# Kernel tuning notes

Measured on AMD Instinct MI355X. Metric: run time of the kernel, lower is better.

## Reference

```python
import jax, jax.numpy as jnp
import numpy as np
from math import gamma, comb

D_POLY = 4
OFFSET = 2
EVAL_MAX = 1.4
N_NODES = 50000
N_EDGES = 800000
IN_FEATS = 256
H_FEATS = 64
NEG_SLOPE = 0.01  # F.leaky_relu / nn.LeakyReLU default


def _beta(a, b):
    return gamma(a) * gamma(b) / gamma(a + b)


def _calculate_theta2(d=D_POLY):
    # Closed-form expansion of sympy poly in calculate_theta2:
    # f(x) = (x/e)^i * (1 - x/e)^(d-i+offset) / (e * Beta(i+1, d+1-i+offset))
    # Returns ascending-order coefficient lists (theta[k] = coeff of x^k).
    e = EVAL_MAX
    thetas = []
    for i in range(OFFSET, d + 1 + OFFSET):
        m = d - i + OFFSET
        B = _beta(i + 1, d + 1 - i + OFFSET)
        c = np.zeros(d + 1 + OFFSET, dtype=np.float64)
        for j in range(m + 1):
            c[i + j] = (1.0 / e) ** i * comb(m, j) * (-1.0 / e) ** j / (e * B)
        thetas.append([float(v) for v in c])
    return thetas


THETAS = _calculate_theta2()


def setup_inputs() -> dict:
    key = jax.random.key(0)
    k1, k2, k3, k4, k5 = jax.random.split(key, 5)
    x = jax.random.normal(k1, (N_NODES, IN_FEATS), dtype=jnp.float32)
    W = jax.random.normal(k2, (IN_FEATS, H_FEATS), dtype=jnp.float32) * 0.05
    b = jax.random.normal(k3, (H_FEATS,), dtype=jnp.float32) * 0.05
    src = jax.random.randint(k4, (N_EDGES,), 0, N_NODES, dtype=jnp.int32)
    dst = jax.random.randint(k5, (N_EDGES,), 0, N_NODES, dtype=jnp.int32)
    return {"x": x, "W": W, "b": b, "src": src, "dst": dst}


def reference(x, W, b, src, dst):
    # BWGNN forward: linear + LeakyReLU, then 5 Beta-wavelet PolyConv filters.
    h = jax.nn.leaky_relu(x @ W + b, NEG_SLOPE)  # [N, H]
    # out_degrees, clamped to 1, then D^{-1/2}
    deg = jax.ops.segment_sum(jnp.ones_like(src, dtype=h.dtype), src, num_segments=N_NODES)
    d_inv = jnp.clip(deg, 1.0) ** -0.5
    d_inv = d_inv[:, None]  # [N, 1]
    outs = []
    for theta in THETAS:
        f = h
        acc = theta[0] * h
        for k in range(1, len(theta)):
            # unnLaplacian: f <- f - D^{-1/2} A^T D^{-1/2} f  (copy_u/sum SpMM)
            msg = jax.ops.segment_sum((f * d_inv)[src], dst, num_segments=N_NODES)
            f = f - msg * d_inv
            acc = acc + theta[k] * f
        outs.append(acc)
    return jnp.concatenate(outs, axis=1)  # [N, 5*H]
```

## Files before the change

### kernel.cpp

```cpp
#include <hip/hip_runtime.h>
#include <math.h>

#define NN 50000
#define NN4 12500
#define NE 800000
#define INF 256
#define HF 64
#define OUTF 320
#define NB4 ((NN4 + 255) / 256)
#define G 128
#define SL (NE / G)

typedef _Float16 half8 __attribute__((ext_vector_type(8)));
typedef float floatx4 __attribute__((ext_vector_type(4)));
typedef float f32x2 __attribute__((ext_vector_type(2)));
typedef float f32x4 __attribute__((ext_vector_type(4)));

static __device__ __forceinline__ unsigned short f2h(float x) {
    _Float16 h = (_Float16)x;
    return *(unsigned short*)&h;
}
static __device__ __forceinline__ float h2f(unsigned short u) {
    _Float16 h = *(_Float16*)&u;
    return (float)h;
}

struct ThetaM { float m[5][7]; };

static void compute_theta(ThetaM& tm) {
    const double e = 1.4;
    auto fact = [](int n) { double r = 1.0; for (int i = 2; i <= n; ++i) r *= i; return r; };
    for (int t = 0; t < 5; ++t) {
        int i = t + 2;
        int mm = 6 - i;
        double B = fact(i) * fact(6 - i) / fact(7);
        for (int k = 0; k < 7; ++k) tm.m[t][k] = 0.f;
        for (int j = 0; j <= mm; ++j) {
            double cb = fact(mm) / (fact(j) * fact(mm - j));
            double v = pow(1.0 / e, (double)i) * cb * pow(-1.0 / e, (double)j) / (e * B);
            tm.m[t][i + j] = (float)v;
        }
    }
}

__global__ __launch_bounds__(64) void zero_kernel(unsigned int* __restrict__ gA,
                                                  unsigned int* __restrict__ gB) {
    if (threadIdx.x < 32) {
        gA[NN * 32 + threadIdx.x] = 0u;
        gB[NN * 32 + threadIdx.x] = 0u;
    }
}

__global__ __launch_bounds__(1024) void hist_kernel(const int* __restrict__ src,
                                                    const int* __restrict__ dst,
                                                    unsigned int* __restrict__ hist_dst,
                                                    unsigned int* __restrict__ hist_src) {
    __shared__ unsigned int h[NN4];
    int b = blockIdx.x;
    const int* arr = (b < G) ? dst : src;
    unsigned int* outp = (b < G) ? hist_dst : hist_src;
    int bb = (b < G) ? b : b - G;
    for (int i = threadIdx.x; i < NN4; i += 1024) h[i] = 0u;
    __syncthreads();
    int base = bb * SL;
    for (int i = threadIdx.x; i < SL; i += 1024) {
        int d = arr[base + i];
        atomicAdd(&h[d >> 2], 1u << ((d & 3) * 8));
    }
    __syncthreads();
    unsigned int* out32 = outp + (size_t)bb * NN4;
    for (int i = threadIdx.x; i < NN4; i += 1024) out32[i] = h[i];
}

__global__ __launch_bounds__(256) void merge_kernel(unsigned int* __restrict__ hist_dst,
                                                    const unsigned int* __restrict__ hist_src,
                                                    int* __restrict__ cnt,
                                                    float* __restrict__ dinv,
                                                    int* __restrict__ partial) {
    __shared__ int s[256];
    int tid = threadIdx.x;
    int t = blockIdx.x * 256 + tid;
    int run0 = 0, run1 = 0, run2 = 0, run3 = 0;
    if (t < NN4) {
        for (int b = 0; b < G; ++b) {
            size_t idx = (size_t)b * NN4 + t;
            unsigned int u = hist_dst[idx];
            hist_dst[idx] = (unsigned int)run0 | ((unsigned int)run1 << 8) |
                            ((unsigned int)run2 << 16) | ((unsigned int)run3 << 24);
            run0 += u & 255u; run1 += (u >> 8) & 255u;
            run2 += (u >> 16) & 255u; run3 += u >> 24;
        }
        *(int4*)&cnt[4 * t] = make_int4(run0, run1, run2, run3);
        int d0 = 0, d1 = 0, d2 = 0, d3 = 0;
        for (int b = 0; b < G; ++b) {
            unsigned int u = hist_src[(size_t)b * NN4 + t];
            d0 += u & 255u; d1 += (u >> 8) & 255u;
            d2 += (u >> 16) & 255u; d3 += u >> 24;
        }
        float e0 = (float)(d0 < 1 ? 1 : d0);
        float e1 = (float)(d1 < 1 ? 1 : d1);
        float e2 = (float)(d2 < 1 ? 1 : d2);
        float e3 = (float)(d3 < 1 ? 1 : d3);
        *(float4*)&dinv[4 * t] = make_float4(1.0f / sqrtf(e0), 1.0f / sqrtf(e1),
                                             1.0f / sqrtf(e2), 1.0f / sqrtf(e3));
    }
    int pad = ((run0 + 3) & ~3) + ((run1 + 3) & ~3) + ((run2 + 3) & ~3) + ((run3 + 3) & ~3);
    s[tid] = pad;
    __syncthreads();
    for (int off = 128; off > 0; off >>= 1) {
        if (tid < off) s[tid] += s[tid + off];
        __syncthreads();
    }
    if (tid == 0) partial[blockIdx.x] = s[0];
}

__global__ __launch_bounds__(256) void scan_partials_kernel(const int* __restrict__ partial,
                                                            int* __restrict__ offsets,
                                                            int* __restrict__ row_ptr) {
    __shared__ int s[256];
    int tid = threadIdx.x;
    s[tid] = (tid < NB4) ? partial[tid] : 0;
    __syncthreads();
    for (int off = 1; off < 256; off <<= 1) {
        int t = (tid >= off) ? s[tid - off] : 0;
        __syncthreads();
        s[tid] += t;
        __syncthreads();
    }
    if (tid < NB4) offsets[tid] = (tid == 0) ? 0 : s[tid - 1];
    if (tid == NB4 - 1) row_ptr[NN] = s[tid];
}

__global__ __launch_bounds__(256) void scan_write_kernel(const int* __restrict__ cnt,
                                                         const int* __restrict__ offsets,
                                                         int* __restrict__ row_ptr,
                                                         int* __restrict__ col) {
    __shared__ int s[256];
    int tid = threadIdx.x;
    int t = blockIdx.x * 256 + tid;
    int4 c = make_int4(0, 0, 0, 0);
    if (t < NN4) c = *(const int4*)&cnt[4 * t];
    int p0 = (c.x + 3) & ~3, p1 = (c.y + 3) & ~3, p2 = (c.z + 3) & ~3, p3 = (c.w + 3) & ~3;
    int csum = p0 + p1 + p2 + p3;
    s[tid] = csum;
    __syncthreads();
    for (int off = 1; off < 256; off <<= 1) {
        int v = (tid >= off) ? s[tid - off] : 0;
        __syncthreads();
        s[tid] += v;
        __syncthreads();
    }
    if (t < NN4) {
        int b0 = offsets[blockIdx.x] + s[tid] - csum;
        int b1 = b0 + p0, b2 = b1 + p1, b3 = b2 + p2;
        *(int4*)&row_ptr[4 * t] = make_int4(b0, b1, b2, b3);
        for (int k = c.x; k < p0; ++k) col[b0 + k] = NN;
        for (int k = c.y; k < p1; ++k) col[b1 + k] = NN;
        for (int k = c.z; k < p2; ++k) col[b2 + k] = NN;
        for (int k = c.w; k < p3; ++k) col[b3 + k] = NN;
    }
}

__global__ __launch_bounds__(1024) void fill_kernel(const int* __restrict__ src,
                                                    const int* __restrict__ dst,
                                                    const unsigned char* __restrict__ hist8,
                                                    const int* __restrict__ row_ptr,
                                                    int* __restrict__ col) {
    __shared__ unsigned int cur[NN4];
    int b = blockIdx.x;
    for (int i = threadIdx.x; i < NN4; i += 1024) cur[i] = 0u;
    __syncthreads();
    int base = b * SL;
    const unsigned char* hrow = hist8 + (size_t)b * NN;
    for (int i = threadIdx.x; i < SL; i += 1024) {
        int d = dst[base + i];
        int sh = (d & 3) * 8;
        unsigned int old = atomicAdd(&cur[d >> 2], 1u << sh);
        int rank = (int)((old >> sh) & 255u);
        int pos = row_ptr[d] + (int)hrow[d] + rank;
        col[pos] = src[base + i];
    }
}

__global__ __launch_bounds__(256) void wprep_kernel(const float* __restrict__ W,
                                                    unsigned short* __restrict__ Wt) {
    int id = blockIdx.x * 256 + threadIdx.x;
    if (id >= HF * INF) return;
    int n = id >> 8;
    int k = id & 255;
    Wt[id] = f2h(W[k * HF + n]);
}

__global__ __launch_bounds__(256) void gemm_kernel(const float* __restrict__ x,
                                                   const unsigned short* __restrict__ Wt,
                                                   const float* __restrict__ b,
                                                   const float* __restrict__ dinv,
                                                   float* __restrict__ f,
                                                   unsigned short* __restrict__ g) {
    __shared__ _Float16 wls[64 * 264];
    __shared__ _Float16 xls[64 * 136];
    int tid = threadIdx.x;
    int row0 = blockIdx.x * 64;
    int wave = tid >> 6;
    int lane = tid & 63;
    int q = lane >> 4;
    int ln = lane & 15;

    {
        const uint4* wg = (const uint4*)Wt;
        for (int i = 0; i < 8; ++i) {
            int l = tid + i * 256;
            int r = l >> 5, c = l & 31;
            *(uint4*)&wls[r * 264 + c * 8] = wg[l];
        }
    }

    floatx4 acc[4] = {{0.f,0.f,0.f,0.f},{0.f,0.f,0.f,0.f},{0.f,0.f,0.f,0.f},{0.f,0.f,0.f,0.f}};

    for (int ch = 0; ch < 2; ++ch) {
        __syncthreads();
        for (int i = 0; i < 8; ++i) {
            int l = tid + i * 256;
            int r = l >> 5, c4 = (l & 31) * 4;
            int grow = row0 + r;
            f32x4 v = {0.f, 0.f, 0.f, 0.f};
            if (grow < NN) v = __builtin_nontemporal_load((const f32x4*)&x[(size_t)grow * INF + ch * 128 + c4]);
            ushort4 hv;
            hv.x = f2h(v[0]); hv.y = f2h(v[1]); hv.z = f2h(v[2]); hv.w = f2h(v[3]);
            *(ushort4*)&xls[r * 136 + c4] = hv;
        }
        __syncthreads();
        int m = wave * 16 + ln;
        #pragma unroll
        for (int kb4 = 0; kb4 < 4; ++kb4) {
            int kb = kb4 * 32;
            half8 a = *(const half8*)&xls[m * 136 + kb + q * 8];
            int kg = ch * 128 + kb + q * 8;
            #pragma unroll
            for (int t = 0; t < 4; ++t) {
                half8 bb = *(const half8*)&wls[(t * 16 + ln) * 264 + kg];
                acc[t] = __builtin_amdgcn_mfma_f32_16x16x32_f16(a, bb, acc[t], 0, 0, 0);
            }
        }
    }

    float bias[4];
    #pragma unroll
    for (int t = 0; t < 4; ++t) bias[t] = b[t * 16 + ln];
    #pragma unroll
    for (int r = 0; r < 4; ++r) {
        int grow = row0 + wave * 16 + q * 4 + r;
        if (grow < NN) {
            float dv = dinv[grow];
            #pragma unroll
            for (int t = 0; t < 4; ++t) {
                float h = acc[t][r] + bias[t];
                h = (h > 0.f) ? h : 0.01f * h;
                int cidx = t * 16 + ln;
                f[(size_t)grow * HF + cidx] = h;
                g[(size_t)grow * HF + cidx] = f2h(h * dv);
            }
        }
    }
}

__global__ __launch_bounds__(256) void prop_kernel(const int* __restrict__ row_ptr,
                                                   const int* __restrict__ col,
                                                   const float* __restrict__ dinv,
                                                   const unsigned int* __restrict__ g_in,
                                                   const float* __restrict__ f_in, int fin_stride,
                                                   float* __restrict__ f_out, int fout_stride,
                                                   unsigned int* __restrict__ g_out) {
    int gidx = blockIdx.x * 256 + threadIdx.x;
    int wid = gidx >> 5;
    int c2 = threadIdx.x & 31;
    if (wid >= NN) return;
    int j   = row_ptr[wid];
    int end = row_ptr[wid + 1];
    float s0 = 0.f, s1 = 0.f;
    for (; j + 8 <= end; j += 8) {
        int4 ca = *(const int4*)&col[j];
        int4 cb = *(const int4*)&col[j + 4];
        unsigned int u0 = g_in[ca.x * 32 + c2];
        unsigned int u1 = g_in[ca.y * 32 + c2];
        unsigned int u2 = g_in[ca.z * 32 + c2];
        unsigned int u3 = g_in[ca.w * 32 + c2];
        unsigned int u4 = g_in[cb.x * 32 + c2];
        unsigned int u5 = g_in[cb.y * 32 + c2];
        unsigned int u6 = g_in[cb.z * 32 + c2];
        unsigned int u7 = g_in[cb.w * 32 + c2];
        s0 += ((h2f(u0 & 0xFFFF) + h2f(u1 & 0xFFFF)) + (h2f(u2 & 0xFFFF) + h2f(u3 & 0xFFFF)))
            + ((h2f(u4 & 0xFFFF) + h2f(u5 & 0xFFFF)) + (h2f(u6 & 0xFFFF) + h2f(u7 & 0xFFFF)));
        s1 += ((h2f(u0 >> 16) + h2f(u1 >> 16)) + (h2f(u2 >> 16) + h2f(u3 >> 16)))
            + ((h2f(u4 >> 16) + h2f(u5 >> 16)) + (h2f(u6 >> 16) + h2f(u7 >> 16)));
    }
    if (j < end) {
        int4 ca = *(const int4*)&col[j];
        unsigned int u0 = g_in[ca.x * 32 + c2];
        unsigned int u1 = g_in[ca.y * 32 + c2];
        unsigned int u2 = g_in[ca.z * 32 + c2];
        unsigned int u3 = g_in[ca.w * 32 + c2];
        s0 += (h2f(u0 & 0xFFFF) + h2f(u1 & 0xFFFF)) + (h2f(u2 & 0xFFFF) + h2f(u3 & 0xFFFF));
        s1 += (h2f(u0 >> 16) + h2f(u1 >> 16)) + (h2f(u2 >> 16) + h2f(u3 >> 16));
    }
    float dv = dinv[wid];
    f32x2 fv = __builtin_nontemporal_load((const f32x2*)&f_in[(size_t)wid * fin_stride + 2 * c2]);
    float fx = fv[0] - s0 * dv;
    float fy = fv[1] - s1 * dv;
    f32x2 ov; ov[0] = fx; ov[1] = fy;
    __builtin_nontemporal_store(ov, (f32x2*)&f_out[(size_t)wid * fout_stride + 2 * c2]);
    if (g_out) g_out[wid * 32 + c2] = (unsigned int)f2h(fx * dv) | ((unsigned int)f2h(fy * dv) << 16);
}

__global__ __launch_bounds__(256) void final_kernel(float* __restrict__ out, ThetaM tm) {
    int idx = blockIdx.x * 256 + threadIdx.x;
    if (idx >= NN * 32) return;
    int n = idx >> 5;
    int c = (idx & 31) * 2;
    f32x2 v[5];
    #pragma unroll
    for (int j = 0; j < 5; ++j)
        v[j] = __builtin_nontemporal_load((const f32x2*)&out[(size_t)n * OUTF + j * HF + c]);
    #pragma unroll
    for (int t = 0; t < 5; ++t) {
        f32x2 o = {0.f, 0.f};
        #pragma unroll
        for (int j = 0; j < 5; ++j) {
            if (j >= t) { o[0] += tm.m[t][j + 2] * v[j][0]; o[1] += tm.m[t][j + 2] * v[j][1]; }
        }
        __builtin_nontemporal_store(o, (f32x2*)&out[(size_t)n * OUTF + t * HF + c]);
    }
}

extern "C" void kernel_launch(void* const* d_in, const int* in_sizes, int n_in,
                              void* d_out, int out_size, void* d_ws, size_t ws_size,
                              hipStream_t stream) {
    const float* x  = (const float*)d_in[0];
    const float* W  = (const float*)d_in[1];
    const float* b  = (const float*)d_in[2];
    const int* src  = (const int*)d_in[3];
    const int* dst  = (const int*)d_in[4];
    float* out = (float*)d_out;

    char* ws = (char*)d_ws;
    size_t off = 0;
    auto alloc = [&](size_t bytes) -> void* {
        void* p = ws + off;
        off += (bytes + 255) & ~(size_t)255;
        return p;
    };
    unsigned int* hist_dst = (unsigned int*)alloc((size_t)G * NN4 * 4);
    unsigned int* hist_src = (unsigned int*)alloc((size_t)G * NN4 * 4);
    int*   cnt     = (int*)alloc((size_t)NN * 4);
    int*   row_ptr = (int*)alloc((size_t)(NN + 1) * 4);
    int*   partial = (int*)alloc((size_t)NB4 * 4);
    int*   offsets = (int*)alloc((size_t)NB4 * 4);
    float* dinv    = (float*)alloc((size_t)NN * 4);
    int*   col     = (int*)alloc((size_t)(NE + 4 * NN) * 4);
    unsigned short* wt = (unsigned short*)alloc((size_t)HF * INF * 2);
    float* fbuf    = (float*)alloc((size_t)NN * HF * 4);
    unsigned short* gA = (unsigned short*)alloc((size_t)(NN + 1) * HF * 2);
    unsigned short* gB = (unsigned short*)alloc((size_t)(NN + 1) * HF * 2);

    zero_kernel<<<1, 64, 0, stream>>>((unsigned int*)gA, (unsigned int*)gB);
    hist_kernel<<<2 * G, 1024, 0, stream>>>(src, dst, hist_dst, hist_src);
    merge_kernel<<<NB4, 256, 0, stream>>>(hist_dst, hist_src, cnt, dinv, partial);
    scan_partials_kernel<<<1, 256, 0, stream>>>(partial, offsets, row_ptr);
    scan_write_kernel<<<NB4, 256, 0, stream>>>(cnt, offsets, row_ptr, col);
    fill_kernel<<<G, 1024, 0, stream>>>(src, dst, (const unsigned char*)hist_dst, row_ptr, col);
    wprep_kernel<<<(HF * INF + 255) / 256, 256, 0, stream>>>(W, wt);
    gemm_kernel<<<(NN + 63) / 64, 256, 0, stream>>>(x, wt, b, dinv, fbuf, gA);

    const int PB = (NN * 32 + 255) / 256;
    prop_kernel<<<PB, 256, 0, stream>>>(row_ptr, col, dinv, (unsigned int*)gA, fbuf, HF, fbuf, HF, (unsigned int*)gB);
    prop_kernel<<<PB, 256, 0, stream>>>(row_ptr, col, dinv, (unsigned int*)gB, fbuf, HF, out + 0 * HF, OUTF, (unsigned int*)gA);
    prop_kernel<<<PB, 256, 0, stream>>>(row_ptr, col, dinv, (unsigned int*)gA, out + 0 * HF, OUTF, out + 1 * HF, OUTF, (unsigned int*)gB);
    prop_kernel<<<PB, 256, 0, stream>>>(row_ptr, col, dinv, (unsigned int*)gB, out + 1 * HF, OUTF, out + 2 * HF, OUTF, (unsigned int*)gA);
    prop_kernel<<<PB, 256, 0, stream>>>(row_ptr, col, dinv, (unsigned int*)gA, out + 2 * HF, OUTF, out + 3 * HF, OUTF, (unsigned int*)gB);
    prop_kernel<<<PB, 256, 0, stream>>>(row_ptr, col, dinv, (unsigned int*)gB, out + 3 * HF, OUTF, out + 4 * HF, OUTF, nullptr);

    ThetaM tm;
    compute_theta(tm);
    final_kernel<<<(NN * 32 + 255) / 256, 256, 0, stream>>>(out, tm);
}
```

Before: 329.4 us.

## Fuse last propagation with theta combine, pre-scale column indices, pad rows to 8

The last SpMM step is merged into the theta-combination kernel, so the fifth filter output no longer makes a global round trip and one launch is dropped. Column indices are stored pre-multiplied by 32, which removes a multiply per gather. Rows are padded to multiples of 8 so the gather loop has no remainder branch and can prefetch the next index pair. Zeroing of the padding row moves into the histogram kernel. The extra padding adds more dummy gathers and a larger column array.

```diff
diff --git a/kernel.cpp b/kernel.cpp
--- a/kernel.cpp
+++ b/kernel.cpp
@@ -43,20 +43,16 @@
     }
 }
 
-__global__ __launch_bounds__(64) void zero_kernel(unsigned int* __restrict__ gA,
-                                                  unsigned int* __restrict__ gB) {
-    if (threadIdx.x < 32) {
-        gA[NN * 32 + threadIdx.x] = 0u;
-        gB[NN * 32 + threadIdx.x] = 0u;
-    }
-}
-
 __global__ __launch_bounds__(1024) void hist_kernel(const int* __restrict__ src,
                                                     const int* __restrict__ dst,
                                                     unsigned int* __restrict__ hist_dst,
-                                                    unsigned int* __restrict__ hist_src) {
+                                                    unsigned int* __restrict__ hist_src,
+                                                    unsigned int* __restrict__ gA,
+                                                    unsigned int* __restrict__ gB) {
     __shared__ unsigned int h[NN4];
     int b = blockIdx.x;
+    if (b == 0 && threadIdx.x < 32) gA[NN * 32 + threadIdx.x] = 0u;
+    if (b == 1 && threadIdx.x < 32) gB[NN * 32 + threadIdx.x] = 0u;
     const int* arr = (b < G) ? dst : src;
     unsigned int* outp = (b < G) ? hist_dst : hist_src;
     int bb = (b < G) ? b : b - G;
@@ -104,7 +100,7 @@
         *(float4*)&dinv[4 * t] = make_float4(1.0f / sqrtf(e0), 1.0f / sqrtf(e1),
                                              1.0f / sqrtf(e2), 1.0f / sqrtf(e3));
     }
-    int pad = ((run0 + 3) & ~3) + ((run1 + 3) & ~3) + ((run2 + 3) & ~3) + ((run3 + 3) & ~3);
+    int pad = ((run0 + 7) & ~7) + ((run1 + 7) & ~7) + ((run2 + 7) & ~7) + ((run3 + 7) & ~7);
     s[tid] = pad;
     __syncthreads();
     for (int off = 128; off > 0; off >>= 1) {
@@ -140,7 +136,7 @@
     int t = blockIdx.x * 256 + tid;
     int4 c = make_int4(0, 0, 0, 0);
     if (t < NN4) c = *(const int4*)&cnt[4 * t];
-    int p0 = (c.x + 3) & ~3, p1 = (c.y + 3) & ~3, p2 = (c.z + 3) & ~3, p3 = (c.w + 3) & ~3;
+    int p0 = (c.x + 7) & ~7, p1 = (c.y + 7) & ~7, p2 = (c.z + 7) & ~7, p3 = (c.w + 7) & ~7;
     int csum = p0 + p1 + p2 + p3;
     s[tid] = csum;
     __syncthreads();
@@ -154,10 +150,11 @@
         int b0 = offsets[blockIdx.x] + s[tid] - csum;
         int b1 = b0 + p0, b2 = b1 + p1, b3 = b2 + p2;
         *(int4*)&row_ptr[4 * t] = make_int4(b0, b1, b2, b3);
-        for (int k = c.x; k < p0; ++k) col[b0 + k] = NN;
-        for (int k = c.y; k < p1; ++k) col[b1 + k] = NN;
-        for (int k = c.z; k < p2; ++k) col[b2 + k] = NN;
-        for (int k = c.w; k < p3; ++k) col[b3 + k] = NN;
+        const int PH = NN << 5;
+        for (int k = c.x; k < p0; ++k) col[b0 + k] = PH;
+        for (int k = c.y; k < p1; ++k) col[b1 + k] = PH;
+        for (int k = c.z; k < p2; ++k) col[b2 + k] = PH;
+        for (int k = c.w; k < p3; ++k) col[b3 + k] = PH;
     }
 }
 
@@ -178,7 +175,7 @@
         unsigned int old = atomicAdd(&cur[d >> 2], 1u << sh);
         int rank = (int)((old >> sh) & 255u);
         int pos = row_ptr[d] + (int)hrow[d] + rank;
-        col[pos] = src[base + i];
+        col[pos] = src[base + i] << 5;
     }
 }
 
@@ -264,6 +261,22 @@
     }
 }
 
+#define ACC8(ca, cb)                                                           \
+    do {                                                                       \
+        unsigned int u0 = g_in[(unsigned)(ca.x + c2)];                         \
+        unsigned int u1 = g_in[(unsigned)(ca.y + c2)];                         \
+        unsigned int u2 = g_in[(unsigned)(ca.z + c2)];                         \
+        unsigned int u3 = g_in[(unsigned)(ca.w + c2)];                         \
+        unsigned int u4 = g_in[(unsigned)(cb.x + c2)];                         \
+        unsigned int u5 = g_in[(unsigned)(cb.y + c2)];                         \
+        unsigned int u6 = g_in[(unsigned)(cb.z + c2)];                         \
+        unsigned int u7 = g_in[(unsigned)(cb.w + c2)];                         \
+        s0 += ((h2f(u0 & 0xFFFF) + h2f(u1 & 0xFFFF)) + (h2f(u2 & 0xFFFF) + h2f(u3 & 0xFFFF)))  \
+            + ((h2f(u4 & 0xFFFF) + h2f(u5 & 0xFFFF)) + (h2f(u6 & 0xFFFF) + h2f(u7 & 0xFFFF))); \
+        s1 += ((h2f(u0 >> 16) + h2f(u1 >> 16)) + (h2f(u2 >> 16) + h2f(u3 >> 16)))              \
+            + ((h2f(u4 >> 16) + h2f(u5 >> 16)) + (h2f(u6 >> 16) + h2f(u7 >> 16)));             \
+    } while (0)
+
 __global__ __launch_bounds__(256) void prop_kernel(const int* __restrict__ row_ptr,
                                                    const int* __restrict__ col,
                                                    const float* __restrict__ dinv,
@@ -277,34 +290,22 @@
     if (wid >= NN) return;
     int j   = row_ptr[wid];
     int end = row_ptr[wid + 1];
-    float s0 = 0.f, s1 = 0.f;
-    for (; j + 8 <= end; j += 8) {
-        int4 ca = *(const int4*)&col[j];
-        int4 cb = *(const int4*)&col[j + 4];
-        unsigned int u0 = g_in[ca.x * 32 + c2];
-        unsigned int u1 = g_in[ca.y * 32 + c2];
-        unsigned int u2 = g_in[ca.z * 32 + c2];
-        unsigned int u3 = g_in[ca.w * 32 + c2];
-        unsigned int u4 = g_in[cb.x * 32 + c2];
-        unsigned int u5 = g_in[cb.y * 32 + c2];
-        unsigned int u6 = g_in[cb.z * 32 + c2];
-        unsigned int u7 = g_in[cb.w * 32 + c2];
-        s0 += ((h2f(u0 & 0xFFFF) + h2f(u1 & 0xFFFF)) + (h2f(u2 & 0xFFFF) + h2f(u3 & 0xFFFF)))
-            + ((h2f(u4 & 0xFFFF) + h2f(u5 & 0xFFFF)) + (h2f(u6 & 0xFFFF) + h2f(u7 & 0xFFFF)));
-        s1 += ((h2f(u0 >> 16) + h2f(u1 >> 16)) + (h2f(u2 >> 16) + h2f(u3 >> 16)))
-            + ((h2f(u4 >> 16) + h2f(u5 >> 16)) + (h2f(u6 >> 16) + h2f(u7 >> 16)));
-    }
-    if (j < end) {
-        int4 ca = *(const int4*)&col[j];
-        unsigned int u0 = g_in[ca.x * 32 + c2];
-        unsigned int u1 = g_in[ca.y * 32 + c2];
-        unsigned int u2 = g_in[ca.z * 32 + c2];
-        unsigned int u3 = g_in[ca.w * 32 + c2];
-        s0 += (h2f(u0 & 0xFFFF) + h2f(u1 & 0xFFFF)) + (h2f(u2 & 0xFFFF) + h2f(u3 & 0xFFFF));
-        s1 += (h2f(u0 >> 16) + h2f(u1 >> 16)) + (h2f(u2 >> 16) + h2f(u3 >> 16));
-    }
     float dv = dinv[wid];
     f32x2 fv = __builtin_nontemporal_load((const f32x2*)&f_in[(size_t)wid * fin_stride + 2 * c2]);
+    float s0 = 0.f, s1 = 0.f;
+    if (j < end) {
+        const int4* c4p = (const int4*)(col + j);
+        int nit = (end - j) >> 3;
+        int4 ca = c4p[0], cb = c4p[1];
+        c4p += 2;
+        for (int it = 1; it < nit; ++it) {
+            int4 na = c4p[0], nb = c4p[1];
+            c4p += 2;
+            ACC8(ca, cb);
+            ca = na; cb = nb;
+        }
+        ACC8(ca, cb);
+    }
     float fx = fv[0] - s0 * dv;
     float fy = fv[1] - s1 * dv;
     f32x2 ov; ov[0] = fx; ov[1] = fy;
@@ -312,23 +313,47 @@
     if (g_out) g_out[wid * 32 + c2] = (unsigned int)f2h(fx * dv) | ((unsigned int)f2h(fy * dv) << 16);
 }
 
-__global__ __launch_bounds__(256) void final_kernel(float* __restrict__ out, ThetaM tm) {
-    int idx = blockIdx.x * 256 + threadIdx.x;
-    if (idx >= NN * 32) return;
-    int n = idx >> 5;
-    int c = (idx & 31) * 2;
-    f32x2 v[5];
-    #pragma unroll
-    for (int j = 0; j < 5; ++j)
-        v[j] = __builtin_nontemporal_load((const f32x2*)&out[(size_t)n * OUTF + j * HF + c]);
+__global__ __launch_bounds__(256) void prop_final_kernel(const int* __restrict__ row_ptr,
+                                                         const int* __restrict__ col,
+                                                         const float* __restrict__ dinv,
+                                                         const unsigned int* __restrict__ g_in,
+                                                         float* __restrict__ out, ThetaM tm) {
+    int gidx = blockIdx.x * 256 + threadIdx.x;
+    int wid = gidx >> 5;
+    int c2 = threadIdx.x & 31;
+    if (wid >= NN) return;
+    int j   = row_ptr[wid];
+    int end = row_ptr[wid + 1];
+    float dv = dinv[wid];
+    float* orow = out + (size_t)wid * OUTF + 2 * c2;
+    f32x2 v2 = *(const f32x2*)&orow[0 * HF];
+    f32x2 v3 = *(const f32x2*)&orow[1 * HF];
+    f32x2 v4 = *(const f32x2*)&orow[2 * HF];
+    f32x2 v5 = *(const f32x2*)&orow[3 * HF];
+    float s0 = 0.f, s1 = 0.f;
+    if (j < end) {
+        const int4* c4p = (const int4*)(col + j);
+        int nit = (end - j) >> 3;
+        int4 ca = c4p[0], cb = c4p[1];
+        c4p += 2;
+        for (int it = 1; it < nit; ++it) {
+            int4 na = c4p[0], nb = c4p[1];
+            c4p += 2;
+            ACC8(ca, cb);
+            ca = na; cb = nb;
+        }
+        ACC8(ca, cb);
+    }
+    f32x2 v6; v6[0] = v5[0] - s0 * dv; v6[1] = v5[1] - s1 * dv;
+    f32x2 v[5] = {v2, v3, v4, v5, v6};
     #pragma unroll
     for (int t = 0; t < 5; ++t) {
         f32x2 o = {0.f, 0.f};
         #pragma unroll
-        for (int j = 0; j < 5; ++j) {
-            if (j >= t) { o[0] += tm.m[t][j + 2] * v[j][0]; o[1] += tm.m[t][j + 2] * v[j][1]; }
-        }
-        __builtin_nontemporal_store(o, (f32x2*)&out[(size_t)n * OUTF + t * HF + c]);
+        for (int jj = 0; jj < 5; ++jj) {
+            if (jj >= t) { o[0] += tm.m[t][jj + 2] * v[jj][0]; o[1] += tm.m[t][jj + 2] * v[jj][1]; }
+        }
+        __builtin_nontemporal_store(o, (f32x2*)&orow[t * HF]);
     }
 }
 
@@ -356,14 +381,14 @@
     int*   partial = (int*)alloc((size_t)NB4 * 4);
     int*   offsets = (int*)alloc((size_t)NB4 * 4);
     float* dinv    = (float*)alloc((size_t)NN * 4);
-    int*   col     = (int*)alloc((size_t)(NE + 4 * NN) * 4);
+    int*   col     = (int*)alloc((size_t)(NE + 8 * NN) * 4);
     unsigned short* wt = (unsigned short*)alloc((size_t)HF * INF * 2);
     float* fbuf    = (float*)alloc((size_t)NN * HF * 4);
     unsigned short* gA = (unsigned short*)alloc((size_t)(NN + 1) * HF * 2);
     unsigned short* gB = (unsigned short*)alloc((size_t)(NN + 1) * HF * 2);
 
-    zero_kernel<<<1, 64, 0, stream>>>((unsigned int*)gA, (unsigned int*)gB);
-    hist_kernel<<<2 * G, 1024, 0, stream>>>(src, dst, hist_dst, hist_src);
+    hist_kernel<<<2 * G, 1024, 0, stream>>>(src, dst, hist_dst, hist_src,
+                                            (unsigned int*)gA, (unsigned int*)gB);
     merge_kernel<<<NB4, 256, 0, stream>>>(hist_dst, hist_src, cnt, dinv, partial);
     scan_partials_kernel<<<1, 256, 0, stream>>>(partial, offsets, row_ptr);
     scan_write_kernel<<<NB4, 256, 0, stream>>>(cnt, offsets, row_ptr, col);
@@ -371,15 +396,14 @@
     wprep_kernel<<<(HF * INF + 255) / 256, 256, 0, stream>>>(W, wt);
     gemm_kernel<<<(NN + 63) / 64, 256, 0, stream>>>(x, wt, b, dinv, fbuf, gA);
 
+    ThetaM tm;
+    compute_theta(tm);
+
     const int PB = (NN * 32 + 255) / 256;
     prop_kernel<<<PB, 256, 0, stream>>>(row_ptr, col, dinv, (unsigned int*)gA, fbuf, HF, fbuf, HF, (unsigned int*)gB);
     prop_kernel<<<PB, 256, 0, stream>>>(row_ptr, col, dinv, (unsigned int*)gB, fbuf, HF, out + 0 * HF, OUTF, (unsigned int*)gA);
     prop_kernel<<<PB, 256, 0, stream>>>(row_ptr, col, dinv, (unsigned int*)gA, out + 0 * HF, OUTF, out + 1 * HF, OUTF, (unsigned int*)gB);
     prop_kernel<<<PB, 256, 0, stream>>>(row_ptr, col, dinv, (unsigned int*)gB, out + 1 * HF, OUTF, out + 2 * HF, OUTF, (unsigned int*)gA);
     prop_kernel<<<PB, 256, 0, stream>>>(row_ptr, col, dinv, (unsigned int*)gA, out + 2 * HF, OUTF, out + 3 * HF, OUTF, (unsigned int*)gB);
-    prop_kernel<<<PB, 256, 0, stream>>>(row_ptr, col, dinv, (unsigned int*)gB, out + 3 * HF, OUTF, out + 4 * HF, OUTF, nullptr);
-
-    ThetaM tm;
-    compute_theta(tm);
-    final_kernel<<<(NN * 32 + 255) / 256, 256, 0, stream>>>(out, tm);
-}
+    prop_final_kernel<<<PB, 256, 0, stream>>>(row_ptr, col, dinv, (unsigned int*)gB, out, tm);
+}
```

Result: faster. 302.3 us (-8.2%).
